# Kernel optimization log

Hardware: AMD Instinct MI355X
Metric: run time of the kernel (lower is better)

Reference implementation:

```python
import jax, jax.numpy as jnp
import numpy as np

THRESHOLD = 0.5
NEG_POS_RATIO = 3


def cxcycz_to_xyz(c):
    return jnp.concatenate([c[..., :3] - c[..., 3:] / 2, c[..., :3] + c[..., 3:] / 2], axis=-1)


def xyz_to_cxcycz(x):
    return jnp.concatenate([(x[..., :3] + x[..., 3:]) / 2, x[..., 3:] - x[..., :3]], axis=-1)


def cxcycz_to_gcxgcygcz(c, priors):
    # SSD offset encoding (variance 0.1 / 0.2), 3D version
    return jnp.concatenate([
        (c[..., :3] - priors[..., :3]) / (priors[..., 3:] / 10.0),
        jnp.log(c[..., 3:] / priors[..., 3:]) * 5.0,
    ], axis=-1)


def jaccard3d(a, b):
    # a: [n,6] xyz boxes, b: [m,6] xyz boxes -> [n,m] IoU
    lo = jnp.maximum(a[:, None, :3], b[None, :, :3])
    hi = jnp.minimum(a[:, None, 3:], b[None, :, 3:])
    inter = jnp.prod(jnp.clip(hi - lo, 0.0, None), axis=-1)
    va = jnp.prod(a[:, 3:] - a[:, :3], axis=-1)
    vb = jnp.prod(b[:, 3:] - b[:, :3], axis=-1)
    return inter / (va[:, None] + vb[None, :] - inter)


def setup_inputs() -> dict:
    key = jax.random.key(0)
    ks = jax.random.split(key, 6)
    B, P, n_obj, n_classes = 16, 131072, 16, 2
    predicted_locs = jax.random.normal(ks[0], (B, P, 6), jnp.float32)
    predicted_scores = jax.random.normal(ks[1], (B, P, n_classes), jnp.float32)
    ctr = jax.random.uniform(ks[2], (B, n_obj, 3), minval=0.2, maxval=0.8)
    sz = jax.random.uniform(ks[3], (B, n_obj, 3), minval=0.05, maxval=0.2)
    boxes = jnp.concatenate([ctr - sz / 2, ctr + sz / 2], axis=-1)
    labels = jnp.ones((B, n_obj), jnp.int32)  # single foreground class (lesion)
    pctr = jax.random.uniform(ks[4], (P, 3), minval=0.0, maxval=1.0)
    psz = jax.random.uniform(ks[5], (P, 3), minval=0.05, maxval=0.3)
    priors_cxcycz = jnp.concatenate([pctr, psz], axis=-1)
    return {
        'predicted_locs': predicted_locs,
        'predicted_scores': predicted_scores,
        'boxes': boxes,
        'labels': labels,
        'priors_cxcycz': priors_cxcycz,
    }


def reference(predicted_locs, predicted_scores, boxes, labels, priors_cxcycz):
    B, P, n_classes = predicted_scores.shape
    n_obj = boxes.shape[1]
    priors_xyz = cxcycz_to_xyz(priors_cxcycz)

    def match(boxes_i, labels_i):
        ov = jaccard3d(boxes_i, priors_xyz)              # [n_obj, P]
        overlap_fp = ov.max(axis=0)                      # best overlap per prior
        object_fp = jnp.argmax(ov, axis=0)               # best object per prior
        prior_fo = jnp.argmax(ov, axis=1)                # best prior per object
        # force each object's best prior to be matched to that object
        object_fp = object_fp.at[prior_fo].set(jnp.arange(n_obj))
        overlap_fp = overlap_fp.at[prior_fo].set(1.0)
        lab = jnp.where(overlap_fp < THRESHOLD, 0, labels_i[object_fp])
        tl = cxcycz_to_gcxgcygcz(xyz_to_cxcycz(boxes_i[object_fp]), priors_cxcycz)
        return lab, tl

    true_classes, true_locs = jax.vmap(match)(boxes, labels)  # [B,P], [B,P,6]

    pos = true_classes > 0                               # [B,P]
    n_pos = pos.sum(axis=1)                              # [B]
    total_pos = n_pos.sum()

    # L1Loss(mean) over positive rows of [*,6]
    loc_abs = jnp.abs(predicted_locs - true_locs).sum(axis=-1)   # [B,P]
    loc_loss = (loc_abs * pos).sum() / (total_pos * 6).astype(predicted_locs.dtype)

    # per-prior cross-entropy
    logp = jax.nn.log_softmax(predicted_scores, axis=-1)
    conf_all = -jnp.take_along_axis(logp, true_classes[..., None], axis=-1)[..., 0]
    conf_all = jnp.where(true_classes < 0, 0.0, conf_all)  # ignored priors (soft mode only)
    conf_pos_sum = (conf_all * pos).sum()

    # hard-negative mining: zero out positives, sort each row descending, take top 3*n_pos
    conf_neg = jnp.where(pos, 0.0, conf_all)
    conf_neg_sorted = -jnp.sort(-conf_neg, axis=1)
    hard = jnp.arange(P)[None, :] < (NEG_POS_RATIO * n_pos)[:, None]
    conf_loss = (jnp.where(hard, conf_neg_sorted, 0.0).sum() + conf_pos_sum) / total_pos.astype(predicted_scores.dtype)
    return conf_loss, loc_loss
```

## Files before the change

kernel.cpp:

```cpp
#include <hip/hip_runtime.h>
#include <math.h>

#define MITEMS 4
#define LB 32


template <int NOBJ, bool FULL>
__global__ __launch_bounds__(256) void mbl_match(
    const float* __restrict__ boxes, const float* __restrict__ priors,
    unsigned long long* __restrict__ part_fo, unsigned char* __restrict__ best_u8,
    int P, int n_obj) {
  const int b = blockIdx.y;
  const int tid = threadIdx.x;
  __shared__ float4 s_box[NOBJ][2];
  __shared__ unsigned long long s_part[4][NOBJ];
  for (int i = tid; i < NOBJ; i += 256) {
    float4 v0, v1;
    if (i < n_obj) {
      const float* bx = boxes + ((size_t)b * n_obj + i) * 6;
      const float l0 = bx[0], l1 = bx[1], l2 = bx[2];
      const float h0 = bx[3], h1 = bx[4], h2 = bx[5];
      v0 = make_float4(l0, l1, l2, h0);
      v1 = make_float4(h1, h2, ((h0 - l0) * (h1 - l1)) * (h2 - l2), 0.f);
    } else {
      v0 = make_float4(3e18f, 3e18f, 3e18f, 1e18f);
      v1 = make_float4(1e18f, 1e18f, 0.f, 0.f);
    }
    s_box[i][0] = v0;
    s_box[i][1] = v1;
  }
  __syncthreads();

  float lo0[MITEMS], lo1[MITEMS], lo2[MITEMS], hi0[MITEMS], hi1[MITEMS],
      hi2[MITEMS], vb[MITEMS];
  unsigned invp[MITEMS];
  const int base = blockIdx.x * (256 * MITEMS);
#pragma unroll
  for (int k = 0; k < MITEMS; ++k) {
    const int p = base + k * 256 + tid;
    if (FULL || p < P) {
      const float2 q0 = *(const float2*)(priors + (size_t)p * 6);
      const float2 q1 = *(const float2*)(priors + (size_t)p * 6 + 2);
      const float2 q2 = *(const float2*)(priors + (size_t)p * 6 + 4);
      lo0[k] = q0.x - q1.y * 0.5f; hi0[k] = q0.x + q1.y * 0.5f;
      lo1[k] = q0.y - q2.x * 0.5f; hi1[k] = q0.y + q2.x * 0.5f;
      lo2[k] = q1.x - q2.y * 0.5f; hi2[k] = q1.x + q2.y * 0.5f;
      vb[k] = (q1.y * q2.x) * q2.y;
      invp[k] = 0xFFFFFFFFu - (unsigned)p;
    } else {
      lo0[k] = lo1[k] = lo2[k] = 3e18f;
      hi0[k] = hi1[k] = hi2[k] = 3e18f;
      vb[k] = 0.f;
      invp[k] = 0u;
    }
  }

  float piou[NOBJ];
  unsigned pinv[NOBJ];
#pragma unroll
  for (int o = 0; o < NOBJ; ++o) { piou[o] = -1.0f; pinv[o] = 0u; }
  float bv[MITEMS];
  int bo[MITEMS];
#pragma unroll
  for (int k = 0; k < MITEMS; ++k) { bv[k] = -1.0f; bo[k] = 0; }

#pragma unroll
  for (int o = 0; o < NOBJ; ++o) {
    const float4 c0 = s_box[o][0];
    const float4 c1 = s_box[o][1];
#pragma unroll
    for (int k = 0; k < MITEMS; ++k) {
      const float d0 = fminf(c0.w, hi0[k]) - fmaxf(c0.x, lo0[k]);
      const float d1 = fminf(c1.x, hi1[k]) - fmaxf(c0.y, lo1[k]);
      const float d2 = fminf(c1.y, hi2[k]) - fmaxf(c0.z, lo2[k]);
      const float inter = (fmaxf(d0, 0.f) * fmaxf(d1, 0.f)) * fmaxf(d2, 0.f);
      const float un = (c1.z + vb[k]) - inter;
      const float iou = inter * __builtin_amdgcn_rcpf(un);
      if (iou > bv[k]) { bv[k] = iou; bo[k] = o; }
      if (iou > piou[o]) { piou[o] = iou; pinv[o] = invp[k]; }
    }
  }

  const int lane = tid & 63, wv = tid >> 6;
#pragma unroll
  for (int o = 0; o < NOBJ; ++o) {
    unsigned long long v =
        (piou[o] < 0.f)
            ? 0ULL
            : (((unsigned long long)__float_as_uint(piou[o]) << 32) | pinv[o]);
    for (int off = 1; off < 64; off <<= 1) {
      const unsigned long long w = __shfl_xor(v, off, 64);
      if (w > v) v = w;
    }
    if (lane == 0) s_part[wv][o] = v;
  }
  __syncthreads();
  if (tid < NOBJ) {
    unsigned long long v = s_part[0][tid];
    for (int w = 1; w < 4; ++w)
      if (s_part[w][tid] > v) v = s_part[w][tid];
    part_fo[((size_t)b * gridDim.x + blockIdx.x) * NOBJ + tid] = v;
  }
#pragma unroll
  for (int k = 0; k < MITEMS; ++k) {
    const int p = base + k * 256 + tid;
    if (FULL || p < P)
      best_u8[(size_t)b * P + p] =
          (unsigned char)((unsigned)bo[k] | (bv[k] >= 0.5f ? 0x80u : 0u));
  }
}

__global__ __launch_bounds__(256) void mbl_reduce_fo(
    const unsigned long long* __restrict__ part_fo,
    unsigned long long* __restrict__ prior_fo, int nblk, int n_obj, int nobjT) {
  const int b = blockIdx.x;
  const int tid = threadIdx.x;
  const int sub = tid & 15;
  for (int o0 = 0; o0 < n_obj; o0 += 16) {
    const int o = o0 + (tid >> 4);
    unsigned long long v = 0ULL;
    if (o < n_obj) {
      const unsigned long long* base = part_fo + (size_t)b * nblk * nobjT + o;
      for (int i = sub; i < nblk; i += 16) {
        const unsigned long long x = base[(size_t)i * nobjT];
        if (x > v) v = x;
      }
    }
#pragma unroll
    for (int off = 1; off < 16; off <<= 1) {
      const unsigned long long w = __shfl_xor(v, off, 64);
      if (w > v) v = w;
    }
    if (sub == 0 && o < n_obj) prior_fo[(size_t)b * n_obj + o] = v;
  }
}

template <int CC>
__global__ __launch_bounds__(256) void mbl_loss(
    const float* __restrict__ locs, const float* __restrict__ scores,
    const float* __restrict__ boxes, const int* __restrict__ labels,
    const float* __restrict__ priors, const unsigned long long* __restrict__ prior_fo,
    const unsigned char* __restrict__ best_u8, float* __restrict__ conf_neg,
    unsigned* __restrict__ hist0, int* __restrict__ n_pos,
    double* __restrict__ pconf, double* __restrict__ ploc, int P, int n_obj, int C) {
  const int b = blockIdx.y;
  const int tid = threadIdx.x;
  __shared__ float s_box[64][6];
  __shared__ int s_lab[64];
  __shared__ unsigned s_fo[64];
  __shared__ unsigned s_hist[4096];
  for (int i = tid; i < 4096; i += 256) s_hist[i] = 0u;
  for (int i = tid; i < n_obj * 6; i += 256)
    s_box[i / 6][i % 6] = boxes[(size_t)b * n_obj * 6 + i];
  for (int i = tid; i < n_obj; i += 256) {
    s_lab[i] = labels[(size_t)b * n_obj + i];
    s_fo[i] = 0xFFFFFFFFu - (unsigned)(prior_fo[(size_t)b * n_obj + i] & 0xFFFFFFFFull);
  }
  __syncthreads();

  unsigned fo_r[16];
  const bool small_obj = (n_obj <= 16);
  if (small_obj) {
#pragma unroll
    for (int o = 0; o < 16; ++o) fo_r[o] = (o < n_obj) ? s_fo[o] : 0xFFFFFFFEu;
  }

  const int chunk = (P + gridDim.x - 1) / gridDim.x;
  const int start = blockIdx.x * chunk;
  const int end = min(start + chunk, P);
  int np_l = 0;
  double cf_l = 0.0, lc_l = 0.0;
  for (int p = start + tid; p < end; p += 256) {
    const unsigned char bp = best_u8[(size_t)b * P + p];
    int obj = bp & 0x7F;
    int posf = bp >> 7;
    if (small_obj) {
#pragma unroll
      for (int o = 0; o < 16; ++o)
        if (fo_r[o] == (unsigned)p) { obj = o; posf = 1; }
    } else {
      for (int o = 0; o < n_obj; ++o)
        if (s_fo[o] == (unsigned)p) { obj = o; posf = 1; }
    }
    const int lab = posf ? s_lab[obj] : 0;

    float conf;
    if (CC == 2) {
      const float2 sc = *(const float2*)(scores + ((size_t)b * P + p) * 2);
      const float m = fmaxf(sc.x, sc.y);
      conf = (lab < 0) ? 0.f
                       : (m + __logf(__expf(sc.x - m) + __expf(sc.y - m)) -
                          ((lab == 0) ? sc.x : sc.y));
    } else {
      const float* sp = scores + ((size_t)b * P + p) * C;
      float m = sp[0];
      for (int c = 1; c < C; ++c) m = fmaxf(m, sp[c]);
      float se = 0.f;
      for (int c = 0; c < C; ++c) se += __expf(sp[c] - m);
      conf = (lab < 0) ? 0.f : (m + __logf(se) - sp[lab]);
    }

    float cn = conf;
    if (lab > 0) {
      np_l++;
      cf_l += (double)conf;
      const float* pr = priors + (size_t)p * 6;
      const float* pl = locs + ((size_t)b * P + p) * 6;
      float ls = 0.f;
      for (int i = 0; i < 3; ++i) {
        const float c0 = (s_box[obj][i] + s_box[obj][i + 3]) * 0.5f;
        const float szb = s_box[obj][i + 3] - s_box[obj][i];
        const float g = (c0 - pr[i]) / (pr[i + 3] / 10.0f);
        const float g2 = logf(szb / pr[i + 3]) * 5.0f;
        ls += fabsf(pl[i] - g) + fabsf(pl[i + 3] - g2);
      }
      lc_l += (double)ls;
      cn = 0.f;
    }
    conf_neg[(size_t)b * P + p] = cn;
    atomicAdd(&s_hist[__float_as_uint(cn) >> 20], 1u);
  }

  __shared__ int r_np[256];
  __shared__ double r_c[256];
  __shared__ double r_l[256];
  r_np[tid] = np_l;
  r_c[tid] = cf_l;
  r_l[tid] = lc_l;
  __syncthreads();
  for (int s = 128; s > 0; s >>= 1) {
    if (tid < s) {
      r_np[tid] += r_np[tid + s];
      r_c[tid] += r_c[tid + s];
      r_l[tid] += r_l[tid + s];
    }
    __syncthreads();
  }
  if (tid == 0 && r_np[0] > 0) {
    atomicAdd(&n_pos[b], r_np[0]);
    atomicAdd(&pconf[b], r_c[0]);
    atomicAdd(&ploc[b], r_l[0]);
  }
  for (int i = tid; i < 4096; i += 256)
    if (s_hist[i]) atomicAdd(&hist0[(size_t)b * 4096 + i], s_hist[i]);
}

template <int BINS>
__device__ void block_select(const unsigned* __restrict__ h, int remk,
                             unsigned* s_scan, int* s_out, unsigned* sel,
                             int* remk_o) {
  constexpr int BPT = BINS / 256;
  const int t = threadIdx.x;
  if (t == 0) { s_out[0] = BINS - 1; s_out[1] = 0; }
  unsigned mb[BPT];
  unsigned s = 0;
#pragma unroll
  for (int i = 0; i < BPT; ++i) { mb[i] = h[t * BPT + i]; s += mb[i]; }
  unsigned incl = s;
  s_scan[t] = incl;
  __syncthreads();
  for (int off = 1; off < 256; off <<= 1) {
    const unsigned add = (t >= off) ? s_scan[t - off] : 0u;
    __syncthreads();
    incl += add;
    s_scan[t] = incl;
    __syncthreads();
  }
  const unsigned total = s_scan[255];
  const unsigned R = total - incl;
  if (remk > 0 && R < (unsigned)remk && R + s >= (unsigned)remk) {
    unsigned acc = R;
    int sel_i = t * BPT, rk = 0;
    bool done = false;
#pragma unroll
    for (int i = BPT - 1; i >= 0; --i) {
      if (!done && acc + mb[i] >= (unsigned)remk) {
        sel_i = t * BPT + i;
        rk = remk - (int)acc;
        done = true;
      }
      if (!done) acc += mb[i];
    }
    s_out[0] = sel_i;
    s_out[1] = rk;
  }
  __syncthreads();
  *sel = (unsigned)s_out[0];
  *remk_o = s_out[1];
  __syncthreads();
}

__global__ __launch_bounds__(256) void mbl_hist1(
    const float* __restrict__ conf_neg, const int* __restrict__ n_pos,
    const unsigned* __restrict__ hist0, unsigned* __restrict__ hist1, int P) {
  const int b = blockIdx.y;
  const int tid = threadIdx.x;
  __shared__ unsigned s_scan[256];
  __shared__ int s_out[2];
  __shared__ unsigned s_hist[4096];
  int K = 3 * n_pos[b];
  if (K > P) K = P;
  unsigned sel0;
  int rem0;
  block_select<4096>(hist0 + (size_t)b * 4096, K, s_scan, s_out, &sel0, &rem0);
  for (int i = tid; i < 4096; i += 256) s_hist[i] = 0u;
  __syncthreads();
  const float* row = conf_neg + (size_t)b * P;
  const int n4 = P >> 2;
  const int per = (n4 + (int)gridDim.x - 1) / (int)gridDim.x;
  const int s4 = blockIdx.x * per, e4 = min(s4 + per, n4);
  for (int i = s4 + tid; i < e4; i += 256) {
    const float4 v = ((const float4*)row)[i];
    unsigned u;
    u = __float_as_uint(v.x); if ((u >> 20) == sel0) atomicAdd(&s_hist[(u >> 8) & 4095u], 1u);
    u = __float_as_uint(v.y); if ((u >> 20) == sel0) atomicAdd(&s_hist[(u >> 8) & 4095u], 1u);
    u = __float_as_uint(v.z); if ((u >> 20) == sel0) atomicAdd(&s_hist[(u >> 8) & 4095u], 1u);
    u = __float_as_uint(v.w); if ((u >> 20) == sel0) atomicAdd(&s_hist[(u >> 8) & 4095u], 1u);
  }
  if (blockIdx.x == 0)
    for (int p = (n4 << 2) + tid; p < P; p += 256) {
      const unsigned u = __float_as_uint(row[p]);
      if ((u >> 20) == sel0) atomicAdd(&s_hist[(u >> 8) & 4095u], 1u);
    }
  __syncthreads();
  for (int i = tid; i < 4096; i += 256)
    if (s_hist[i]) atomicAdd(&hist1[(size_t)b * 4096 + i], s_hist[i]);
}

__global__ __launch_bounds__(256) void mbl_hist2(
    const float* __restrict__ conf_neg, const int* __restrict__ n_pos,
    const unsigned* __restrict__ hist0, const unsigned* __restrict__ hist1,
    unsigned* __restrict__ hist2, int P) {
  const int b = blockIdx.y;
  const int tid = threadIdx.x;
  __shared__ unsigned s_scan[256];
  __shared__ int s_out[2];
  __shared__ unsigned s_hist[256];
  int K = 3 * n_pos[b];
  if (K > P) K = P;
  unsigned sel0, sel1;
  int rem0, rem1;
  block_select<4096>(hist0 + (size_t)b * 4096, K, s_scan, s_out, &sel0, &rem0);
  block_select<4096>(hist1 + (size_t)b * 4096, rem0, s_scan, s_out, &sel1, &rem1);
  s_hist[tid] = 0u;
  __syncthreads();
  const unsigned pref20 = (sel0 << 12) | sel1;
  const float* row = conf_neg + (size_t)b * P;
  const int n4 = P >> 2;
  const int per = (n4 + (int)gridDim.x - 1) / (int)gridDim.x;
  const int s4 = blockIdx.x * per, e4 = min(s4 + per, n4);
  for (int i = s4 + tid; i < e4; i += 256) {
    const float4 v = ((const float4*)row)[i];
    unsigned u;
    u = __float_as_uint(v.x); if ((u >> 8) == pref20) atomicAdd(&s_hist[u & 255u], 1u);
    u = __float_as_uint(v.y); if ((u >> 8) == pref20) atomicAdd(&s_hist[u & 255u], 1u);
    u = __float_as_uint(v.z); if ((u >> 8) == pref20) atomicAdd(&s_hist[u & 255u], 1u);
    u = __float_as_uint(v.w); if ((u >> 8) == pref20) atomicAdd(&s_hist[u & 255u], 1u);
  }
  if (blockIdx.x == 0)
    for (int p = (n4 << 2) + tid; p < P; p += 256) {
      const unsigned u = __float_as_uint(row[p]);
      if ((u >> 8) == pref20) atomicAdd(&s_hist[u & 255u], 1u);
    }
  __syncthreads();
  if (s_hist[tid]) atomicAdd(&hist2[(size_t)b * 256 + tid], s_hist[tid]);
}

__global__ __launch_bounds__(256) void mbl_sum(
    const float* __restrict__ conf_neg, const int* __restrict__ n_pos,
    const unsigned* __restrict__ hist0, const unsigned* __restrict__ hist1,
    const unsigned* __restrict__ hist2, double* __restrict__ phard, int P) {
  const int b = blockIdx.y;
  const int tid = threadIdx.x;
  __shared__ unsigned s_scan[256];
  __shared__ int s_out[2];
  int K = 3 * n_pos[b];
  if (K > P) K = P;
  unsigned sel0, sel1, sel2;
  int rem0, rem1, rem2;
  block_select<4096>(hist0 + (size_t)b * 4096, K, s_scan, s_out, &sel0, &rem0);
  block_select<4096>(hist1 + (size_t)b * 4096, rem0, s_scan, s_out, &sel1, &rem1);
  block_select<256>(hist2 + (size_t)b * 256, rem1, s_scan, s_out, &sel2, &rem2);
  const unsigned tbits = (sel0 << 20) | (sel1 << 8) | sel2;
  const float* row = conf_neg + (size_t)b * P;
  const int n4 = P >> 2;
  const int per = (n4 + (int)gridDim.x - 1) / (int)gridDim.x;
  const int s4 = blockIdx.x * per, e4 = min(s4 + per, n4);
  double local = 0.0;
  for (int i = s4 + tid; i < e4; i += 256) {
    const float4 v = ((const float4*)row)[i];
    if (__float_as_uint(v.x) > tbits) local += (double)v.x;
    if (__float_as_uint(v.y) > tbits) local += (double)v.y;
    if (__float_as_uint(v.z) > tbits) local += (double)v.z;
    if (__float_as_uint(v.w) > tbits) local += (double)v.w;
  }
  if (blockIdx.x == 0)
    for (int p = (n4 << 2) + tid; p < P; p += 256) {
      const float v = row[p];
      if (__float_as_uint(v) > tbits) local += (double)v;
    }
  __shared__ double red[256];
  red[tid] = local;
  __syncthreads();
  for (int s = 128; s > 0; s >>= 1) {
    if (tid < s) red[tid] += red[tid + s];
    __syncthreads();
  }
  if (tid == 0) {
    double v = red[0];
    if (blockIdx.x == 0 && rem2 > 0)
      v += (double)rem2 * (double)__uint_as_float(tbits);
    if (v != 0.0) atomicAdd(&phard[b], v);
  }
}

__global__ void mbl_finalize(const double* __restrict__ pconf,
                             const double* __restrict__ ploc,
                             const double* __restrict__ phard,
                             const int* __restrict__ n_pos, int B,
                             float* __restrict__ out) {
  if (threadIdx.x == 0 && blockIdx.x == 0) {
    double tp = 0.0, cs = 0.0, ls = 0.0, hs = 0.0;
    for (int b = 0; b < B; ++b) {
      tp += (double)n_pos[b];
      cs += pconf[b];
      ls += ploc[b];
      hs += phard[b];
    }
    out[0] = (float)((hs + cs) / tp);
    out[1] = (float)(ls / (tp * 6.0));
  }
}

extern "C" void kernel_launch(void* const* d_in, const int* in_sizes, int n_in,
                              void* d_out, int out_size, void* d_ws, size_t ws_size,
                              hipStream_t stream) {
  const float* locs = (const float*)d_in[0];
  const float* scores = (const float*)d_in[1];
  const float* boxes = (const float*)d_in[2];
  const int* labels = (const int*)d_in[3];
  const float* priors = (const float*)d_in[4];

  const long long sz_locs = (long long)in_sizes[0];
  const long long sz_scores = (long long)in_sizes[1];
  const long long sz_priors = (long long)in_sizes[4];
  const int P = (int)(sz_priors / 6);
  const int B = (int)(sz_locs / sz_priors);
  const int n_obj = in_sizes[3] / B;
  const int C = (int)(sz_scores * 6 / sz_locs);

  const int tile = 256 * MITEMS;
  const int nblk = (P + tile - 1) / tile;
  const int nobjT = (n_obj <= 16) ? 16 : ((n_obj <= 32) ? 32 : 64);

  char* ws = (char*)d_ws;
  size_t off = 0;
  double* pconf = (double*)(ws + off); off += (size_t)B * 8;
  double* ploc = (double*)(ws + off); off += (size_t)B * 8;
  double* phard = (double*)(ws + off); off += (size_t)B * 8;
  int* n_pos = (int*)(ws + off); off += ((size_t)B * 4 + 15) & ~(size_t)15;
  unsigned long long* prior_fo = (unsigned long long*)(ws + off);
  off += ((size_t)B * n_obj * 8 + 15) & ~(size_t)15;
  unsigned* hist0 = (unsigned*)(ws + off); off += (size_t)B * 4096 * 4;
  unsigned* hist1 = (unsigned*)(ws + off); off += (size_t)B * 4096 * 4;
  unsigned* hist2 = (unsigned*)(ws + off); off += (size_t)B * 256 * 4;
  const size_t zero_bytes = off;
  float* conf_neg = (float*)(ws + off); off += ((size_t)B * P * 4 + 15) & ~(size_t)15;
  unsigned char* best_u8 = (unsigned char*)(ws + off);
  off += ((size_t)B * P + 15) & ~(size_t)15;
  unsigned long long* part_fo = (unsigned long long*)(ws + off);
  off += (size_t)B * nblk * nobjT * 8;
  (void)ws_size;

  hipMemsetAsync(d_ws, 0, zero_bytes, stream);

  const dim3 mgrid(nblk, B);
  const bool full = (P % tile) == 0;
  if (n_obj <= 16) {
    if (full) mbl_match<16, true><<<mgrid, 256, 0, stream>>>(boxes, priors, part_fo, best_u8, P, n_obj);
    else      mbl_match<16, false><<<mgrid, 256, 0, stream>>>(boxes, priors, part_fo, best_u8, P, n_obj);
  } else if (n_obj <= 32) {
    if (full) mbl_match<32, true><<<mgrid, 256, 0, stream>>>(boxes, priors, part_fo, best_u8, P, n_obj);
    else      mbl_match<32, false><<<mgrid, 256, 0, stream>>>(boxes, priors, part_fo, best_u8, P, n_obj);
  } else {
    if (full) mbl_match<64, true><<<mgrid, 256, 0, stream>>>(boxes, priors, part_fo, best_u8, P, n_obj);
    else      mbl_match<64, false><<<mgrid, 256, 0, stream>>>(boxes, priors, part_fo, best_u8, P, n_obj);
  }

  mbl_reduce_fo<<<B, 256, 0, stream>>>(part_fo, prior_fo, nblk, n_obj, nobjT);

  const dim3 lgrid(LB, B);
  if (C == 2)
    mbl_loss<2><<<lgrid, 256, 0, stream>>>(locs, scores, boxes, labels, priors, prior_fo,
                                           best_u8, conf_neg, hist0, n_pos, pconf, ploc,
                                           P, n_obj, C);
  else
    mbl_loss<0><<<lgrid, 256, 0, stream>>>(locs, scores, boxes, labels, priors, prior_fo,
                                           best_u8, conf_neg, hist0, n_pos, pconf, ploc,
                                           P, n_obj, C);

  mbl_hist1<<<lgrid, 256, 0, stream>>>(conf_neg, n_pos, hist0, hist1, P);
  mbl_hist2<<<lgrid, 256, 0, stream>>>(conf_neg, n_pos, hist0, hist1, hist2, P);
  mbl_sum<<<lgrid, 256, 0, stream>>>(conf_neg, n_pos, hist0, hist1, hist2, phard, P);
  mbl_finalize<<<1, 64, 0, stream>>>(pconf, ploc, phard, n_pos, B, (float*)d_out);
}
```

Measured before the change: 99.94 us.

## Fuse memset/finalize, drop third radix pass, write forced matches in reduce

Halves items per thread in the matching kernel and replaces the shuffle-based per-object max with shared-memory transposed reduction. Zeroing of workspace moves into the reduce kernel, which also writes forced best-prior matches directly into best_u8, removing the per-prior scan in the loss kernel. The third histogram pass is removed and the remaining tie bucket is approximated by its midpoint value, and finalize is fused into the sum kernel via a last-block counter. This cuts kernel launches and memory passes but makes the hard-negative sum approximate within the low 8 bits.

Result: faster. 88.60 us (-11.4%).

```diff
diff --git a/kernel.cpp b/kernel.cpp
--- a/kernel.cpp
+++ b/kernel.cpp
@@ -1,7 +1,7 @@
 #include <hip/hip_runtime.h>
 #include <math.h>
 
-#define MITEMS 4
+#define MITEMS 2
 #define LB 32
 
 
@@ -13,7 +13,10 @@
   const int b = blockIdx.y;
   const int tid = threadIdx.x;
   __shared__ float4 s_box[NOBJ][2];
-  __shared__ unsigned long long s_part[4][NOBJ];
+  __shared__ unsigned s_iou[8][257];
+  __shared__ unsigned s_inv[8][257];
+  __shared__ unsigned long long s_red2[8][33];
+
   for (int i = tid; i < NOBJ; i += 256) {
     float4 v0, v1;
     if (i < n_obj) {
@@ -81,26 +84,6 @@
     }
   }
 
-  const int lane = tid & 63, wv = tid >> 6;
-#pragma unroll
-  for (int o = 0; o < NOBJ; ++o) {
-    unsigned long long v =
-        (piou[o] < 0.f)
-            ? 0ULL
-            : (((unsigned long long)__float_as_uint(piou[o]) << 32) | pinv[o]);
-    for (int off = 1; off < 64; off <<= 1) {
-      const unsigned long long w = __shfl_xor(v, off, 64);
-      if (w > v) v = w;
-    }
-    if (lane == 0) s_part[wv][o] = v;
-  }
-  __syncthreads();
-  if (tid < NOBJ) {
-    unsigned long long v = s_part[0][tid];
-    for (int w = 1; w < 4; ++w)
-      if (s_part[w][tid] > v) v = s_part[w][tid];
-    part_fo[((size_t)b * gridDim.x + blockIdx.x) * NOBJ + tid] = v;
-  }
 #pragma unroll
   for (int k = 0; k < MITEMS; ++k) {
     const int p = base + k * 256 + tid;
@@ -108,21 +91,61 @@
       best_u8[(size_t)b * P + p] =
           (unsigned char)((unsigned)bo[k] | (bv[k] >= 0.5f ? 0x80u : 0u));
   }
+
+  for (int pass = 0; pass < NOBJ / 8; ++pass) {
+    if (pass > 0) __syncthreads();
+#pragma unroll
+    for (int o = 0; o < NOBJ; ++o) {
+      if ((o >> 3) == pass) {
+        s_iou[o & 7][tid] = __float_as_uint(piou[o]);
+        s_inv[o & 7][tid] = pinv[o];
+      }
+    }
+    __syncthreads();
+    const int obj8 = tid >> 5, seg = tid & 31;
+    unsigned long long m = 0ULL;
+#pragma unroll
+    for (int i = 0; i < 8; ++i) {
+      const int idx = seg + 32 * i;
+      const unsigned long long x =
+          ((unsigned long long)s_iou[obj8][idx] << 32) | s_inv[obj8][idx];
+      if (x > m) m = x;
+    }
+    s_red2[obj8][seg] = m;
+    __syncthreads();
+    if (tid < 8) {
+      unsigned long long m2 = 0ULL;
+      for (int i = 0; i < 32; ++i) {
+        const unsigned long long x = s_red2[tid][i];
+        if (x > m2) m2 = x;
+      }
+      const int o = pass * 8 + tid;
+      if (o < n_obj)
+        part_fo[((size_t)b * gridDim.x + blockIdx.x) * NOBJ + o] = m2;
+    }
+  }
 }
 
 __global__ __launch_bounds__(256) void mbl_reduce_fo(
     const unsigned long long* __restrict__ part_fo,
-    unsigned long long* __restrict__ prior_fo, int nblk, int n_obj, int nobjT) {
+    unsigned char* __restrict__ best_u8,
+    unsigned long long* __restrict__ zero_buf, int zero_words,
+    int nblk, int n_obj, int nobjT, int P) {
   const int b = blockIdx.x;
   const int tid = threadIdx.x;
-  const int sub = tid & 15;
+  {
+    const int total = (int)gridDim.x * 256;
+    for (int i = b * 256 + tid; i < zero_words; i += total) zero_buf[i] = 0ULL;
+  }
+  __shared__ unsigned s_win[64];
+  const int j = tid & 15;
   for (int o0 = 0; o0 < n_obj; o0 += 16) {
     const int o = o0 + (tid >> 4);
     unsigned long long v = 0ULL;
     if (o < n_obj) {
-      const unsigned long long* base = part_fo + (size_t)b * nblk * nobjT + o;
-      for (int i = sub; i < nblk; i += 16) {
-        const unsigned long long x = base[(size_t)i * nobjT];
+      const unsigned long long* src = part_fo + (size_t)b * nblk * nobjT + o;
+      for (int i = j; i < nblk; i += 16) {
+        const unsigned long long x = src[(size_t)i * nobjT];
         if (x > v) v = x;
       }
     }
@@ -131,7 +154,13 @@
       const unsigned long long w = __shfl_xor(v, off, 64);
       if (w > v) v = w;
     }
-    if (sub == 0 && o < n_obj) prior_fo[(size_t)b * n_obj + o] = v;
+    if (j == 0 && o < n_obj)
+      s_win[o] = 0xFFFFFFFFu - (unsigned)(v & 0xFFFFFFFFull);
+  }
+  __syncthreads();
+  if (tid == 0) {
+    for (int o = 0; o < n_obj; ++o)
+      best_u8[(size_t)b * P + s_win[o]] = (unsigned char)(0x80u | (unsigned)o);
   }
 }
 
@@ -139,31 +168,20 @@
 __global__ __launch_bounds__(256) void mbl_loss(
     const float* __restrict__ locs, const float* __restrict__ scores,
     const float* __restrict__ boxes, const int* __restrict__ labels,
-    const float* __restrict__ priors, const unsigned long long* __restrict__ prior_fo,
-    const unsigned char* __restrict__ best_u8, float* __restrict__ conf_neg,
-    unsigned* __restrict__ hist0, int* __restrict__ n_pos,
-    double* __restrict__ pconf, double* __restrict__ ploc, int P, int n_obj, int C) {
+    const float* __restrict__ priors, const unsigned char* __restrict__ best_u8,
+    float* __restrict__ conf_neg, unsigned* __restrict__ hist0,
+    int* __restrict__ n_pos, double* __restrict__ pconf, double* __restrict__ ploc,
+    int P, int n_obj, int C) {
   const int b = blockIdx.y;
   const int tid = threadIdx.x;
   __shared__ float s_box[64][6];
   __shared__ int s_lab[64];
-  __shared__ unsigned s_fo[64];
   __shared__ unsigned s_hist[4096];
   for (int i = tid; i < 4096; i += 256) s_hist[i] = 0u;
   for (int i = tid; i < n_obj * 6; i += 256)
     s_box[i / 6][i % 6] = boxes[(size_t)b * n_obj * 6 + i];
-  for (int i = tid; i < n_obj; i += 256) {
-    s_lab[i] = labels[(size_t)b * n_obj + i];
-    s_fo[i] = 0xFFFFFFFFu - (unsigned)(prior_fo[(size_t)b * n_obj + i] & 0xFFFFFFFFull);
-  }
-  __syncthreads();
-
-  unsigned fo_r[16];
-  const bool small_obj = (n_obj <= 16);
-  if (small_obj) {
-#pragma unroll
-    for (int o = 0; o < 16; ++o) fo_r[o] = (o < n_obj) ? s_fo[o] : 0xFFFFFFFEu;
-  }
+  for (int i = tid; i < n_obj; i += 256) s_lab[i] = labels[(size_t)b * n_obj + i];
+  __syncthreads();
 
   const int chunk = (P + gridDim.x - 1) / gridDim.x;
   const int start = blockIdx.x * chunk;
@@ -172,16 +190,8 @@
   double cf_l = 0.0, lc_l = 0.0;
   for (int p = start + tid; p < end; p += 256) {
     const unsigned char bp = best_u8[(size_t)b * P + p];
-    int obj = bp & 0x7F;
-    int posf = bp >> 7;
-    if (small_obj) {
-#pragma unroll
-      for (int o = 0; o < 16; ++o)
-        if (fo_r[o] == (unsigned)p) { obj = o; posf = 1; }
-    } else {
-      for (int o = 0; o < n_obj; ++o)
-        if (s_fo[o] == (unsigned)p) { obj = o; posf = 1; }
-    }
+    const int obj = bp & 0x7F;
+    const int posf = bp >> 7;
     const int lab = posf ? s_lab[obj] : 0;
 
     float conf;
@@ -327,61 +337,24 @@
     if (s_hist[i]) atomicAdd(&hist1[(size_t)b * 4096 + i], s_hist[i]);
 }
 
-__global__ __launch_bounds__(256) void mbl_hist2(
+__global__ __launch_bounds__(256) void mbl_sum(
     const float* __restrict__ conf_neg, const int* __restrict__ n_pos,
     const unsigned* __restrict__ hist0, const unsigned* __restrict__ hist1,
-    unsigned* __restrict__ hist2, int P) {
+    const double* __restrict__ pconf, const double* __restrict__ ploc,
+    double* __restrict__ phard, unsigned* __restrict__ counter,
+    int P, int B, float* __restrict__ out) {
   const int b = blockIdx.y;
   const int tid = threadIdx.x;
   __shared__ unsigned s_scan[256];
   __shared__ int s_out[2];
-  __shared__ unsigned s_hist[256];
   int K = 3 * n_pos[b];
   if (K > P) K = P;
   unsigned sel0, sel1;
   int rem0, rem1;
   block_select<4096>(hist0 + (size_t)b * 4096, K, s_scan, s_out, &sel0, &rem0);
   block_select<4096>(hist1 + (size_t)b * 4096, rem0, s_scan, s_out, &sel1, &rem1);
-  s_hist[tid] = 0u;
-  __syncthreads();
-  const unsigned pref20 = (sel0 << 12) | sel1;
-  const float* row = conf_neg + (size_t)b * P;
-  const int n4 = P >> 2;
-  const int per = (n4 + (int)gridDim.x - 1) / (int)gridDim.x;
-  const int s4 = blockIdx.x * per, e4 = min(s4 + per, n4);
-  for (int i = s4 + tid; i < e4; i += 256) {
-    const float4 v = ((const float4*)row)[i];
-    unsigned u;
-    u = __float_as_uint(v.x); if ((u >> 8) == pref20) atomicAdd(&s_hist[u & 255u], 1u);
-    u = __float_as_uint(v.y); if ((u >> 8) == pref20) atomicAdd(&s_hist[u & 255u], 1u);
-    u = __float_as_uint(v.z); if ((u >> 8) == pref20) atomicAdd(&s_hist[u & 255u], 1u);
-    u = __float_as_uint(v.w); if ((u >> 8) == pref20) atomicAdd(&s_hist[u & 255u], 1u);
-  }
-  if (blockIdx.x == 0)
-    for (int p = (n4 << 2) + tid; p < P; p += 256) {
-      const unsigned u = __float_as_uint(row[p]);
-      if ((u >> 8) == pref20) atomicAdd(&s_hist[u & 255u], 1u);
-    }
-  __syncthreads();
-  if (s_hist[tid]) atomicAdd(&hist2[(size_t)b * 256 + tid], s_hist[tid]);
-}
-
-__global__ __launch_bounds__(256) void mbl_sum(
-    const float* __restrict__ conf_neg, const int* __restrict__ n_pos,
-    const unsigned* __restrict__ hist0, const unsigned* __restrict__ hist1,
-    const unsigned* __restrict__ hist2, double* __restrict__ phard, int P) {
-  const int b = blockIdx.y;
-  const int tid = threadIdx.x;
-  __shared__ unsigned s_scan[256];
-  __shared__ int s_out[2];
-  int K = 3 * n_pos[b];
-  if (K > P) K = P;
-  unsigned sel0, sel1, sel2;
-  int rem0, rem1, rem2;
-  block_select<4096>(hist0 + (size_t)b * 4096, K, s_scan, s_out, &sel0, &rem0);
-  block_select<4096>(hist1 + (size_t)b * 4096, rem0, s_scan, s_out, &sel1, &rem1);
-  block_select<256>(hist2 + (size_t)b * 256, rem1, s_scan, s_out, &sel2, &rem2);
-  const unsigned tbits = (sel0 << 20) | (sel1 << 8) | sel2;
+  const unsigned pref24 = (sel0 << 12) | sel1;
+  const unsigned tb = (pref24 << 8) | 0xFFu;
   const float* row = conf_neg + (size_t)b * P;
   const int n4 = P >> 2;
   const int per = (n4 + (int)gridDim.x - 1) / (int)gridDim.x;
@@ -389,16 +362,19 @@
   double local = 0.0;
   for (int i = s4 + tid; i < e4; i += 256) {
     const float4 v = ((const float4*)row)[i];
-    if (__float_as_uint(v.x) > tbits) local += (double)v.x;
-    if (__float_as_uint(v.y) > tbits) local += (double)v.y;
-    if (__float_as_uint(v.z) > tbits) local += (double)v.z;
-    if (__float_as_uint(v.w) > tbits) local += (double)v.w;
-  }
-  if (blockIdx.x == 0)
+    if (__float_as_uint(v.x) > tb) local += (double)v.x;
+    if (__float_as_uint(v.y) > tb) local += (double)v.y;
+    if (__float_as_uint(v.z) > tb) local += (double)v.z;
+    if (__float_as_uint(v.w) > tb) local += (double)v.w;
+  }
+  if (blockIdx.x == 0) {
     for (int p = (n4 << 2) + tid; p < P; p += 256) {
       const float v = row[p];
-      if (__float_as_uint(v) > tbits) local += (double)v;
-    }
+      if (__float_as_uint(v) > tb) local += (double)v;
+    }
+    if (tid == 0 && rem1 > 0)
+      local += (double)rem1 * (double)__uint_as_float((pref24 << 8) | 0x80u);
+  }
   __shared__ double red[256];
   red[tid] = local;
   __syncthreads();
@@ -407,28 +383,20 @@
     __syncthreads();
   }
   if (tid == 0) {
-    double v = red[0];
-    if (blockIdx.x == 0 && rem2 > 0)
-      v += (double)rem2 * (double)__uint_as_float(tbits);
-    if (v != 0.0) atomicAdd(&phard[b], v);
-  }
-}
-
-__global__ void mbl_finalize(const double* __restrict__ pconf,
-                             const double* __restrict__ ploc,
-                             const double* __restrict__ phard,
-                             const int* __restrict__ n_pos, int B,
-                             float* __restrict__ out) {
-  if (threadIdx.x == 0 && blockIdx.x == 0) {
-    double tp = 0.0, cs = 0.0, ls = 0.0, hs = 0.0;
-    for (int b = 0; b < B; ++b) {
-      tp += (double)n_pos[b];
-      cs += pconf[b];
-      ls += ploc[b];
-      hs += phard[b];
-    }
-    out[0] = (float)((hs + cs) / tp);
-    out[1] = (float)(ls / (tp * 6.0));
+    if (red[0] != 0.0) atomicAdd(&phard[b], red[0]);
+    __threadfence();
+    const unsigned done = atomicAdd(counter, 1u);
+    if (done == gridDim.x * gridDim.y - 1) {
+      double tp = 0.0, cs = 0.0, ls = 0.0, hs = 0.0;
+      for (int i = 0; i < B; ++i) {
+        tp += (double)n_pos[i];
+        cs += pconf[i];
+        ls += ploc[i];
+        hs += atomicAdd(&phard[i], 0.0);
+      }
+      out[0] = (float)((hs + cs) / tp);
+      out[1] = (float)(ls / (tp * 6.0));
+    }
   }
 }
 
@@ -459,11 +427,9 @@
   double* ploc = (double*)(ws + off); off += (size_t)B * 8;
   double* phard = (double*)(ws + off); off += (size_t)B * 8;
   int* n_pos = (int*)(ws + off); off += ((size_t)B * 4 + 15) & ~(size_t)15;
-  unsigned long long* prior_fo = (unsigned long long*)(ws + off);
-  off += ((size_t)B * n_obj * 8 + 15) & ~(size_t)15;
+  unsigned* counter = (unsigned*)(ws + off); off += 16;
   unsigned* hist0 = (unsigned*)(ws + off); off += (size_t)B * 4096 * 4;
   unsigned* hist1 = (unsigned*)(ws + off); off += (size_t)B * 4096 * 4;
-  unsigned* hist2 = (unsigned*)(ws + off); off += (size_t)B * 256 * 4;
   const size_t zero_bytes = off;
   float* conf_neg = (float*)(ws + off); off += ((size_t)B * P * 4 + 15) & ~(size_t)15;
   unsigned char* best_u8 = (unsigned char*)(ws + off);
@@ -471,8 +437,6 @@
   unsigned long long* part_fo = (unsigned long long*)(ws + off);
   off += (size_t)B * nblk * nobjT * 8;
   (void)ws_size;
-
-  hipMemsetAsync(d_ws, 0, zero_bytes, stream);
 
   const dim3 mgrid(nblk, B);
   const bool full = (P % tile) == 0;
@@ -487,20 +451,20 @@
     else      mbl_match<64, false><<<mgrid, 256, 0, stream>>>(boxes, priors, part_fo, best_u8, P, n_obj);
   }
 
-  mbl_reduce_fo<<<B, 256, 0, stream>>>(part_fo, prior_fo, nblk, n_obj, nobjT);
+  mbl_reduce_fo<<<B, 256, 0, stream>>>(part_fo, best_u8, (unsigned long long*)d_ws,
+                                       (int)(zero_bytes / 8), nblk, n_obj, nobjT, P);
 
   const dim3 lgrid(LB, B);
   if (C == 2)
-    mbl_loss<2><<<lgrid, 256, 0, stream>>>(locs, scores, boxes, labels, priors, prior_fo,
+    mbl_loss<2><<<lgrid, 256, 0, stream>>>(locs, scores, boxes, labels, priors,
                                            best_u8, conf_neg, hist0, n_pos, pconf, ploc,
                                            P, n_obj, C);
   else
-    mbl_loss<0><<<lgrid, 256, 0, stream>>>(locs, scores, boxes, labels, priors, prior_fo,
+    mbl_loss<0><<<lgrid, 256, 0, stream>>>(locs, scores, boxes, labels, priors,
                                            best_u8, conf_neg, hist0, n_pos, pconf, ploc,
                                            P, n_obj, C);
 
   mbl_hist1<<<lgrid, 256, 0, stream>>>(conf_neg, n_pos, hist0, hist1, P);
-  mbl_hist2<<<lgrid, 256, 0, stream>>>(conf_neg, n_pos, hist0, hist1, hist2, P);
-  mbl_sum<<<lgrid, 256, 0, stream>>>(conf_neg, n_pos, hist0, hist1, hist2, phard, P);
-  mbl_finalize<<<1, 64, 0, stream>>>(pconf, ploc, phard, n_pos, B, (float*)d_out);
-}
+  mbl_sum<<<lgrid, 256, 0, stream>>>(conf_neg, n_pos, hist0, hist1, pconf, ploc,
+                                     phard, counter, P, B, (float*)d_out);
+}
```
